# Kernel tuning notes

Hardware: AMD Instinct MI355X
Metric: run time of the kernel (lower is better)

Reference implementation:

```python
import jax, jax.numpy as jnp
import numpy as np

S, B, D, H, L = 1024, 2, 1024, 16, 4
HD = D // H            # 64
MLP = 4 * D            # 4096
EPS = 1e-5


def _ln(x, w, b):
    m = x.mean(-1, keepdims=True)
    v = ((x - m) ** 2).mean(-1, keepdims=True)
    return (x - m) * jax.lax.rsqrt(v + EPS) * w + b


def _rotate_half(x):
    h = x.shape[-1] // 2
    return jnp.concatenate([-x[..., h:], x[..., :h]], axis=-1)


def _rope(t, cos, sin):
    # t: (B, S, H, HD); cos/sin: (S, HD) broadcast to (1, S, 1, HD)
    return t * cos[None, :, None, :] + _rotate_half(t) * sin[None, :, None, :]


def setup_inputs() -> dict:
    key = jax.random.key(0)
    ks = iter(jax.random.split(key, 64))

    def p(shape, scale=0.02):
        return jax.random.normal(next(ks), shape, jnp.float32) * scale

    return {
        "x": jax.random.normal(next(ks), (S, B, D), jnp.float32),
        "rotary_pos_emb": jax.random.normal(next(ks), (S, HD // 2), jnp.float32),
        # stacked per-layer params (leading dim L) for lax.scan
        "ln1_w": jnp.ones((L, D), jnp.float32), "ln1_b": jnp.zeros((L, D), jnp.float32),
        "in_w": p((L, 3 * D, D)), "in_b": jnp.zeros((L, 3 * D), jnp.float32),
        "out_w": p((L, D, D)), "out_b": jnp.zeros((L, D), jnp.float32),
        "ln2_w": jnp.ones((L, D), jnp.float32), "ln2_b": jnp.zeros((L, D), jnp.float32),
        "fc_w": p((L, MLP, D)), "fc_b": jnp.zeros((L, MLP), jnp.float32),
        "cp_w": p((L, D, MLP)), "cp_b": jnp.zeros((L, D), jnp.float32),
        # attention pooling head (qkv_bias=False in CrossAttention)
        "pn_q_w": jnp.ones((D,), jnp.float32), "pn_q_b": jnp.zeros((D,), jnp.float32),
        "pn_k_w": jnp.ones((D,), jnp.float32), "pn_k_b": jnp.zeros((D,), jnp.float32),
        "pn_v_w": jnp.ones((D,), jnp.float32), "pn_v_b": jnp.zeros((D,), jnp.float32),
        "pq_w": p((D, D)), "pk_w": p((D, D)), "pv_w": p((D, D)),
        "pp_w": p((D, D)), "pp_b": jnp.zeros((D,), jnp.float32),
    }


def reference(x, rotary_pos_emb, ln1_w, ln1_b, in_w, in_b, out_w, out_b,
              ln2_w, ln2_b, fc_w, fc_b, cp_w, cp_b,
              pn_q_w, pn_q_b, pn_k_w, pn_k_b, pn_v_w, pn_v_b,
              pq_w, pk_w, pv_w, pp_w, pp_b):
    # freqs (S, HD/2) -> cos/sin tiled twice along last dim: (S, HD)
    cos = jnp.tile(jnp.cos(rotary_pos_emb), (1, 2))
    sin = jnp.tile(jnp.sin(rotary_pos_emb), (1, 2))
    scale = 1.0 / np.sqrt(HD).astype(np.float32)

    def layer(h, p):
        l1w, l1b, iw, ib, ow, ob, l2w, l2b, fw, fb, cw, cb = p
        a = _ln(h, l1w, l1b)
        qkv = jnp.einsum('sbd,ed->sbe', a, iw) + ib           # (S,B,3D)
        qkv = qkv.reshape(S, B, 3, H, HD)
        q = jnp.transpose(qkv[:, :, 0], (1, 0, 2, 3))          # (B,S,H,HD)
        k = jnp.transpose(qkv[:, :, 1], (1, 0, 2, 3))
        v = jnp.transpose(qkv[:, :, 2], (1, 0, 2, 3))
        q = _rope(q, cos, sin)
        k = _rope(k, cos, sin)
        q, k, v = (t.transpose(0, 2, 1, 3) for t in (q, k, v))  # (B,H,S,HD)
        attn = jax.nn.softmax(jnp.einsum('bhsd,bhtd->bhst', q, k) * scale, axis=-1)
        o = jnp.einsum('bhst,bhtd->bhsd', attn, v)
        o = o.transpose(2, 0, 1, 3).reshape(S, B, D)           # back to (S,B,D)
        h = h + jnp.einsum('sbd,ed->sbe', o, ow) + ob          # residual + out_proj
        m = _ln(h, l2w, l2b)
        m = jax.nn.gelu(jnp.einsum('sbd,ed->sbe', m, fw) + fb, approximate=False)
        h = h + jnp.einsum('sbe,de->sbd', m, cw) + cb          # residual + c_proj
        return h, None

    h, _ = jax.lax.scan(layer, x, (ln1_w, ln1_b, in_w, in_b, out_w, out_b,
                                   ln2_w, ln2_b, fc_w, fc_b, cp_w, cp_b))

    # AttentionPoolingBlock: mean-pooled single query, cross-attend over tokens
    t = h.transpose(1, 0, 2)                                   # (B,N,C)
    xq = _ln(t.mean(1, keepdims=True), pn_q_w, pn_q_b)         # (B,1,C)
    xk = _ln(t, pn_k_w, pn_k_b)
    xv = _ln(t, pn_v_w, pn_v_b)
    q = (xq @ pq_w.T).reshape(B, 1, H, HD).transpose(0, 2, 1, 3)   # (B,H,1,HD)
    k = (xk @ pk_w.T).reshape(B, S, H, HD).transpose(0, 2, 1, 3)
    v = (xv @ pv_w.T).reshape(B, S, H, HD).transpose(0, 2, 1, 3)
    a = jax.nn.softmax(jnp.einsum('bhqd,bhtd->bhqt', q, k) * scale, axis=-1)
    o = jnp.einsum('bhqt,bhtd->bhqd', a, v).transpose(0, 2, 1, 3).reshape(B, 1, D)
    return (o @ pp_w.T + pp_b)[:, 0]                           # (B, D)
```

## Files before the change

### kernel.cpp

```cpp
#include <hip/hip_runtime.h>
#include <math.h>

#define S_LEN  1024
#define BATCH  2
#define DMODEL 1024
#define NHEAD  16
#define HDIM   64
#define NLAYER 4
#define MLPD   4096
#define MROWS  (S_LEN*BATCH)

typedef __attribute__((ext_vector_type(8))) short bf16x8_t;
typedef __attribute__((ext_vector_type(4))) float f32x4_t;

__device__ __forceinline__ unsigned short f2bf(float f) {
  union { float f; unsigned u; } c; c.f = f;
  return (unsigned short)((c.u + 0x7FFFu + ((c.u >> 16) & 1u)) >> 16);
}
__device__ __forceinline__ float bf2f(unsigned short u) {
  union { unsigned u; float f; } c; c.u = ((unsigned)u) << 16; return c.f;
}

__device__ __forceinline__ void gl_lds16(const unsigned short* g, unsigned short* l) {
  __builtin_amdgcn_global_load_lds(
      (const __attribute__((address_space(1))) unsigned int*)(g),
      (__attribute__((address_space(3))) unsigned int*)(l), 16, 0, 0);
}

__global__ __launch_bounds__(256) void w2bf_kernel(const float* __restrict__ src,
    unsigned short* __restrict__ dst, int n) {
  const int i = (blockIdx.x * 256 + threadIdx.x) * 8;
  if (i >= n) return;
  float4 v0 = *(const float4*)(src + i);
  float4 v1 = *(const float4*)(src + i + 4);
  ushort4 u0, u1;
  u0.x = f2bf(v0.x); u0.y = f2bf(v0.y); u0.z = f2bf(v0.z); u0.w = f2bf(v0.w);
  u1.x = f2bf(v1.x); u1.y = f2bf(v1.y); u1.z = f2bf(v1.z); u1.w = f2bf(v1.w);
  *(ushort4*)(dst + i)     = u0;
  *(ushort4*)(dst + i + 4) = u1;
}

__global__ __launch_bounds__(256) void trig_kernel(const float* __restrict__ rot,
    float2* __restrict__ tab) {
  const int i = blockIdx.x * 256 + threadIdx.x;
  const float f = rot[i];
  tab[i] = make_float2(cosf(f), sinf(f));
}

template<bool BF16OUT>
__global__ __launch_bounds__(256) void ln_kernel(const float* __restrict__ x,
    const float* __restrict__ w, const float* __restrict__ b,
    void* __restrict__ out, float inscale) {
  const int row = blockIdx.x;
  const int tid = threadIdx.x;
  const float* xr = x + (size_t)row * DMODEL;
  float4 v = *(const float4*)(xr + tid * 4);
  v.x *= inscale; v.y *= inscale; v.z *= inscale; v.w *= inscale;
  float s1 = v.x + v.y + v.z + v.w;
  float s2 = v.x*v.x + v.y*v.y + v.z*v.z + v.w*v.w;
  #pragma unroll
  for (int off = 32; off; off >>= 1) {
    s1 += __shfl_xor(s1, off);
    s2 += __shfl_xor(s2, off);
  }
  __shared__ float as1[4], as2[4];
  if ((tid & 63) == 0) { as1[tid >> 6] = s1; as2[tid >> 6] = s2; }
  __syncthreads();
  s1 = as1[0] + as1[1] + as1[2] + as1[3];
  s2 = as2[0] + as2[1] + as2[2] + as2[3];
  const float mean = s1 * (1.0f / DMODEL);
  const float var  = s2 * (1.0f / DMODEL) - mean * mean;
  const float r = rsqrtf(var + 1e-5f);
  float4 wv = *(const float4*)(w + tid * 4);
  float4 bv = *(const float4*)(b + tid * 4);
  float o0 = (v.x - mean) * r * wv.x + bv.x;
  float o1 = (v.y - mean) * r * wv.y + bv.y;
  float o2 = (v.z - mean) * r * wv.z + bv.z;
  float o3 = (v.w - mean) * r * wv.w + bv.w;
  if (BF16OUT) {
    ushort4 u; u.x = f2bf(o0); u.y = f2bf(o1); u.z = f2bf(o2); u.w = f2bf(o3);
    *(ushort4*)((unsigned short*)out + (size_t)row * DMODEL + tid * 4) = u;
  } else {
    float4 ov; ov.x = o0; ov.y = o1; ov.z = o2; ov.w = o3;
    *(float4*)((float*)out + (size_t)row * DMODEL + tid * 4) = ov;
  }
}

template<int NS, bool ADDDEST, bool DOLN>
__global__ __launch_bounds__(256) void reduce_ln_kernel(
    const float* __restrict__ part, const float* __restrict__ bias,
    float* __restrict__ dest, const float* __restrict__ lnw,
    const float* __restrict__ lnb, unsigned short* __restrict__ lnout) {
  const int row = blockIdx.x;
  const int tid = threadIdx.x;
  const size_t off = (size_t)row * DMODEL + tid * 4;
  float4 v;
  if (ADDDEST) v = *(const float4*)(dest + off);
  else { v.x = 0.f; v.y = 0.f; v.z = 0.f; v.w = 0.f; }
  if (bias) {
    float4 b4 = *(const float4*)(bias + tid * 4);
    v.x += b4.x; v.y += b4.y; v.z += b4.z; v.w += b4.w;
  }
  #pragma unroll
  for (int z = 0; z < NS; ++z) {
    float4 p = *(const float4*)(part + (size_t)z * (MROWS * DMODEL) + off);
    v.x += p.x; v.y += p.y; v.z += p.z; v.w += p.w;
  }
  *(float4*)(dest + off) = v;
  if (DOLN) {
    float s1 = v.x + v.y + v.z + v.w;
    float s2 = v.x*v.x + v.y*v.y + v.z*v.z + v.w*v.w;
    #pragma unroll
    for (int o = 32; o; o >>= 1) {
      s1 += __shfl_xor(s1, o);
      s2 += __shfl_xor(s2, o);
    }
    __shared__ float as1[4], as2[4];
    if ((tid & 63) == 0) { as1[tid >> 6] = s1; as2[tid >> 6] = s2; }
    __syncthreads();
    s1 = as1[0] + as1[1] + as1[2] + as1[3];
    s2 = as2[0] + as2[1] + as2[2] + as2[3];
    const float mean = s1 * (1.0f / DMODEL);
    const float var  = s2 * (1.0f / DMODEL) - mean * mean;
    const float r = rsqrtf(var + 1e-5f);
    float4 wv = *(const float4*)(lnw + tid * 4);
    float4 bv = *(const float4*)(lnb + tid * 4);
    ushort4 u;
    u.x = f2bf((v.x - mean) * r * wv.x + bv.x);
    u.y = f2bf((v.y - mean) * r * wv.y + bv.y);
    u.z = f2bf((v.z - mean) * r * wv.z + bv.z);
    u.w = f2bf((v.w - mean) * r * wv.w + bv.w);
    *(ushort4*)(lnout + (size_t)row * DMODEL + tid * 4) = u;
  }
}

template<int SPLIT, bool GELU, bool PARTIAL, bool OUTBF16>
__global__ __launch_bounds__(256, 3) void gemm_mfma(
    const unsigned short* __restrict__ A, const unsigned short* __restrict__ W,
    const float* __restrict__ bias, void* __restrict__ Cout,
    int M, int N, int K) {
  constexpr int BK = 32;
  __shared__ __align__(16) unsigned short As[3][128 * BK];
  __shared__ __align__(16) unsigned short Bs[3][128 * BK];
  const int tid  = threadIdx.x;
  const int wid  = tid >> 6;
  const int lane = tid & 63;
  const int lrow = lane & 15;
  const int lq   = lane >> 4;

  const int NB = gridDim.x, MB = gridDim.y;
  const int f = blockIdx.y * NB + blockIdx.x;
  const int xcd = f & 7;
  const int idx = f >> 3;
  const int m0 = (idx % MB) * 128;
  const int n0 = (xcd + (idx / MB) * 8) * 128;

  const int wm = (wid >> 1) * 64;
  const int wn = (wid & 1) * 64;
  const int Kc = K / SPLIT;
  const int kbase = blockIdx.z * Kc;
  const int nt = Kc / BK;

  f32x4_t acc[4][4];
  #pragma unroll
  for (int i = 0; i < 4; ++i)
    #pragma unroll
    for (int j = 0; j < 4; ++j) acc[i][j] = (f32x4_t){0.f, 0.f, 0.f, 0.f};

  const int c1 = tid, c2 = tid + 256;
  const unsigned short* Ag1 = A + (size_t)(m0 + (c1 >> 2)) * K + kbase + (c1 & 3) * 8;
  const unsigned short* Ag2 = A + (size_t)(m0 + (c2 >> 2)) * K + kbase + (c2 & 3) * 8;
  const unsigned short* Wg1 = W + (size_t)(n0 + (c1 >> 2)) * K + kbase + (c1 & 3) * 8;
  const unsigned short* Wg2 = W + (size_t)(n0 + (c2 >> 2)) * K + kbase + (c2 & 3) * 8;
  const int l1 = c1 * 8, l2 = c2 * 8;

  auto stage = [&](int t, int b) {
    const int ko = t * BK;
    gl_lds16(Ag1 + ko, &As[b][l1]);
    gl_lds16(Ag2 + ko, &As[b][l2]);
    gl_lds16(Wg1 + ko, &Bs[b][l1]);
    gl_lds16(Wg2 + ko, &Bs[b][l2]);
  };
  auto compute = [&](int b) {
    bf16x8_t af[4], bfr[4];
    #pragma unroll
    for (int i = 0; i < 4; ++i)
      af[i] = *(const bf16x8_t*)&As[b][(wm + i * 16 + lrow) * BK + lq * 8];
    #pragma unroll
    for (int j = 0; j < 4; ++j)
      bfr[j] = *(const bf16x8_t*)&Bs[b][(wn + j * 16 + lrow) * BK + lq * 8];
    #pragma unroll
    for (int i = 0; i < 4; ++i)
      #pragma unroll
      for (int j = 0; j < 4; ++j)
        acc[i][j] = __builtin_amdgcn_mfma_f32_16x16x32_bf16(af[i], bfr[j], acc[i][j], 0, 0, 0);
  };

  stage(0, 0);
  stage(1, 1);

  int cr = 0;
  int cs = 2;
  for (int t = 0; t < nt - 1; ++t) {
    asm volatile("s_waitcnt vmcnt(4)" ::: "memory");
    __builtin_amdgcn_sched_barrier(0);
    __builtin_amdgcn_s_barrier();
    __builtin_amdgcn_sched_barrier(0);
    if (t + 2 < nt) stage(t + 2, cs);
    compute(cr);
    cr = (cr == 2) ? 0 : cr + 1;
    cs = (cs == 2) ? 0 : cs + 1;
  }
  asm volatile("s_waitcnt vmcnt(0)" ::: "memory");
  __builtin_amdgcn_sched_barrier(0);
  __builtin_amdgcn_s_barrier();
  __builtin_amdgcn_sched_barrier(0);
  compute(cr);

  const size_t zoff = PARTIAL ? (size_t)blockIdx.z * ((size_t)M * N) : 0;
  float bj[4];
  #pragma unroll
  for (int j = 0; j < 4; ++j)
    bj[j] = (bias && (SPLIT == 1 || blockIdx.z == 0)) ? bias[n0 + wn + j * 16 + lrow] : 0.f;
  #pragma unroll
  for (int i = 0; i < 4; ++i) {
    #pragma unroll
    for (int r = 0; r < 4; ++r) {
      const int row = m0 + wm + i * 16 + lq * 4 + r;
      const size_t idx2 = (size_t)row * N + n0 + wn + lrow;
      #pragma unroll
      for (int j = 0; j < 4; ++j) {
        float val = acc[i][j][r] + bj[j];
        if (GELU)
          val = 0.5f * val * (1.0f + erff(val * 0.70710678118654752f));
        if (PARTIAL)
          ((float*)Cout)[zoff + idx2 + j * 16] = val;
        else if (OUTBF16)
          ((unsigned short*)Cout)[idx2 + j * 16] = f2bf(val);
        else
          ((float*)Cout)[idx2 + j * 16] = val;
      }
    }
  }
}

__global__ __launch_bounds__(256) void rope_kernel(const unsigned short* __restrict__ qkv,
    const float2* __restrict__ trig, unsigned short* __restrict__ qt,
    unsigned short* __restrict__ kt, unsigned short* __restrict__ vt) {
  const int idx = blockIdx.x * 256 + threadIdx.x;
  const int d  = idx & 63;
  const int hh = (idx >> 6) & 15;
  const int m  = idx >> 10;
  const int s  = m >> 1;
  const int b  = m & 1;
  const float2 t = trig[s * 32 + (d & 31)];
  const float cs = t.x;
  const float sn = t.y;
  const float sign = (d < 32) ? -1.0f : 1.0f;
  const size_t base  = (size_t)m * 3072 + hh * 64;
  const int bh = b * 16 + hh;
  const size_t obase = (((size_t)bh * 1024 + s) << 6) + d;
  float qv = bf2f(qkv[base + d]);
  float qp = bf2f(qkv[base + (d ^ 32)]);
  qt[obase] = f2bf(qv * cs + sign * qp * sn);
  float kv = bf2f(qkv[base + 1024 + d]);
  float kp = bf2f(qkv[base + 1024 + (d ^ 32)]);
  kt[obase] = f2bf(kv * cs + sign * kp * sn);
  vt[(((size_t)bh * 64 + d) << 10) + s] = qkv[base + 2048 + d];
}

__global__ __launch_bounds__(256, 3) void attn_kernel(
    const unsigned short* __restrict__ q, const unsigned short* __restrict__ k,
    const unsigned short* __restrict__ vtr, unsigned short* __restrict__ o) {
  const int tid  = threadIdx.x;
  const int wid  = tid >> 6;
  const int lane = tid & 63;
  const int col  = lane & 15;
  const int quad = lane >> 4;
  const int bh   = blockIdx.x >> 4;
  const int qw   = (blockIdx.x & 15) * 64 + wid * 16;

  __shared__ __align__(16) unsigned short Ks[64 * 72];
  __shared__ __align__(16) unsigned short Vs[64 * 72];
  __shared__ __align__(16) unsigned short Pl_[4][16 * 72];
  unsigned short* Pl = Pl_[wid];

  const unsigned short* kb = k   + ((size_t)bh << 16);
  const unsigned short* vb = vtr + ((size_t)bh << 16);

  bf16x8_t qa0, qa1;
  {
    const unsigned short* qp = q + ((((size_t)bh << 10) + qw + col) << 6) + quad * 8;
    qa0 = *(const bf16x8_t*)(qp);
    qa1 = *(const bf16x8_t*)(qp + 32);
  }

  f32x4_t oacc[4];
  #pragma unroll
  for (int j = 0; j < 4; ++j) oacc[j] = (f32x4_t){0.f, 0.f, 0.f, 0.f};
  float mr[4] = {-3.0e38f, -3.0e38f, -3.0e38f, -3.0e38f};
  float lr[4] = {0.f, 0.f, 0.f, 0.f};

  const int srow = tid >> 2;
  const int scol = (tid & 3) * 16;
  const unsigned short* gk0 = kb + (size_t)srow * 64 + scol;
  const unsigned short* gv0 = vb + (size_t)srow * 1024 + scol;
  unsigned short* lk0 = &Ks[srow * 72 + scol];
  unsigned short* lv0 = &Vs[srow * 72 + scol];

  {
    uint4 ka = *(const uint4*)(gk0);
    uint4 kc = *(const uint4*)(gk0 + 8);
    uint4 va = *(const uint4*)(gv0);
    uint4 vc = *(const uint4*)(gv0 + 8);
    *(uint4*)(lk0)     = ka;
    *(uint4*)(lk0 + 8) = kc;
    *(uint4*)(lv0)     = va;
    *(uint4*)(lv0 + 8) = vc;
  }
  __syncthreads();

  for (int t0 = 0; t0 < 1024; t0 += 64) {
    const bool more = (t0 + 64) < 1024;
    uint4 nka, nkc, nva, nvc;
    if (more) {
      const unsigned short* gk = gk0 + (size_t)(t0 + 64) * 64;
      const unsigned short* gv = gv0 + (t0 + 64);
      nka = *(const uint4*)(gk);
      nkc = *(const uint4*)(gk + 8);
      nva = *(const uint4*)(gv);
      nvc = *(const uint4*)(gv + 8);
    }

    f32x4_t sc[4];
    #pragma unroll
    for (int j = 0; j < 4; ++j) {
      bf16x8_t kf0 = *(const bf16x8_t*)&Ks[(j * 16 + col) * 72 + quad * 8];
      bf16x8_t kf1 = *(const bf16x8_t*)&Ks[(j * 16 + col) * 72 + quad * 8 + 32];
      f32x4_t c = (f32x4_t){0.f, 0.f, 0.f, 0.f};
      c = __builtin_amdgcn_mfma_f32_16x16x32_bf16(qa0, kf0, c, 0, 0, 0);
      c = __builtin_amdgcn_mfma_f32_16x16x32_bf16(qa1, kf1, c, 0, 0, 0);
      sc[j] = c;
    }

    #pragma unroll
    for (int r = 0; r < 4; ++r) {
      float s0 = sc[0][r] * 0.125f, s1 = sc[1][r] * 0.125f;
      float s2 = sc[2][r] * 0.125f, s3 = sc[3][r] * 0.125f;
      float rm = fmaxf(fmaxf(s0, s1), fmaxf(s2, s3));
      rm = fmaxf(rm, __shfl_xor(rm, 1));
      rm = fmaxf(rm, __shfl_xor(rm, 2));
      rm = fmaxf(rm, __shfl_xor(rm, 4));
      rm = fmaxf(rm, __shfl_xor(rm, 8));
      const float mn = fmaxf(mr[r], rm);
      const float alpha = __expf(mr[r] - mn);
      mr[r] = mn;
      const float p0 = __expf(s0 - mn), p1 = __expf(s1 - mn);
      const float p2 = __expf(s2 - mn), p3 = __expf(s3 - mn);
      float rs = p0 + p1 + p2 + p3;
      rs += __shfl_xor(rs, 1);
      rs += __shfl_xor(rs, 2);
      rs += __shfl_xor(rs, 4);
      rs += __shfl_xor(rs, 8);
      lr[r] = lr[r] * alpha + rs;
      #pragma unroll
      for (int j = 0; j < 4; ++j) oacc[j][r] *= alpha;
      const int prow = (quad * 4 + r) * 72;
      Pl[prow +  0 + col] = f2bf(p0);
      Pl[prow + 16 + col] = f2bf(p1);
      Pl[prow + 32 + col] = f2bf(p2);
      Pl[prow + 48 + col] = f2bf(p3);
    }

    bf16x8_t pa0 = *(const bf16x8_t*)&Pl[col * 72 + quad * 8];
    bf16x8_t pa1 = *(const bf16x8_t*)&Pl[col * 72 + quad * 8 + 32];
    #pragma unroll
    for (int j = 0; j < 4; ++j) {
      bf16x8_t vf0 = *(const bf16x8_t*)&Vs[(j * 16 + col) * 72 + quad * 8];
      bf16x8_t vf1 = *(const bf16x8_t*)&Vs[(j * 16 + col) * 72 + quad * 8 + 32];
      oacc[j] = __builtin_amdgcn_mfma_f32_16x16x32_bf16(pa0, vf0, oacc[j], 0, 0, 0);
      oacc[j] = __builtin_amdgcn_mfma_f32_16x16x32_bf16(pa1, vf1, oacc[j], 0, 0, 0);
    }

    __syncthreads();
    if (more) {
      *(uint4*)(lk0)     = nka;
      *(uint4*)(lk0 + 8) = nkc;
      *(uint4*)(lv0)     = nva;
      *(uint4*)(lv0 + 8) = nvc;
    }
    __syncthreads();
  }

  const int b = bh >> 4, hh = bh & 15;
  #pragma unroll
  for (int r = 0; r < 4; ++r) {
    const float inv = 1.0f / lr[r];
    const int sq = qw + quad * 4 + r;
    unsigned short* orow = o + (((size_t)sq * 2 + b) << 10) + hh * 64;
    #pragma unroll
    for (int j = 0; j < 4; ++j)
      orow[j * 16 + col] = f2bf(oacc[j][r] * inv);
  }
}

__global__ __launch_bounds__(256) void mean_kernel(const float* __restrict__ h,
    float* __restrict__ tsum) {
  const int idx = blockIdx.x * 256 + threadIdx.x;
  const int bd = idx & 2047;
  const int sc = idx >> 11;
  const int b = bd >> 10, d = bd & 1023;
  float sm = 0.f;
  for (int s = sc * 128; s < sc * 128 + 128; ++s)
    sm += h[(((size_t)s * 2 + b) << 10) + d];
  atomicAdd(&tsum[bd], sm);
}

__global__ __launch_bounds__(256) void smallmv_kernel(const float* __restrict__ in,
    const float* __restrict__ W, const float* __restrict__ bias,
    float* __restrict__ out) {
  const int lane = threadIdx.x & 63;
  const int n = blockIdx.x * 4 + (threadIdx.x >> 6);
  const int b = blockIdx.y;
  const float* wr = W + (size_t)n * 1024;
  const float* xr = in + (size_t)b * 1024;
  float sm = 0.f;
  #pragma unroll
  for (int j = 0; j < 4; ++j) {
    float4 wv = *(const float4*)(wr + lane * 4 + j * 256);
    float4 xv = *(const float4*)(xr + lane * 4 + j * 256);
    sm += wv.x * xv.x + wv.y * xv.y + wv.z * xv.z + wv.w * xv.w;
  }
  #pragma unroll
  for (int off = 32; off; off >>= 1) sm += __shfl_xor(sm, off);
  if (lane == 0) out[(size_t)b * 1024 + n] = sm + (bias ? bias[n] : 0.f);
}

__global__ __launch_bounds__(256) void pool_attn_part(const float* __restrict__ q,
    const float* __restrict__ k, const float* __restrict__ v,
    float* __restrict__ part) {
  const int wid  = (blockIdx.x * 256 + threadIdx.x) >> 6;
  const int lane = threadIdx.x & 63;
  const int bh = wid >> 4, kblk = wid & 15;
  const int b = bh >> 4, hh = bh & 15;
  const float qd = q[(size_t)b * 1024 + hh * 64 + lane];
  float mx = -3.0e38f, l = 0.f, acc = 0.f;
  for (int t = kblk * 64; t < kblk * 64 + 64; ++t) {
    const size_t ro = (((size_t)t * 2 + b) << 10) + hh * 64 + lane;
    float p = qd * k[ro];
    p += __shfl_xor(p, 32); p += __shfl_xor(p, 16); p += __shfl_xor(p, 8);
    p += __shfl_xor(p, 4);  p += __shfl_xor(p, 2);  p += __shfl_xor(p, 1);
    const float sc = p * 0.125f;
    const float mn = fmaxf(mx, sc);
    const float alpha = __expf(mx - mn);
    const float w = __expf(sc - mn);
    acc = acc * alpha + w * v[ro];
    l   = l * alpha + w;
    mx  = mn;
  }
  float* pp = part + (size_t)wid * 68;
  if (lane == 0) { pp[0] = mx; pp[1] = l; }
  pp[4 + lane] = acc;
}

__global__ __launch_bounds__(256) void pool_attn_comb(const float* __restrict__ part,
    float* __restrict__ o) {
  const int wid  = (blockIdx.x * 256 + threadIdx.x) >> 6;
  const int lane = threadIdx.x & 63;
  const float* pb = part + (size_t)wid * 16 * 68;
  float M = -3.0e38f;
  #pragma unroll
  for (int w = 0; w < 16; ++w) M = fmaxf(M, pb[w * 68]);
  float L = 0.f, O = 0.f;
  #pragma unroll
  for (int w = 0; w < 16; ++w) {
    const float e = __expf(pb[w * 68] - M);
    L += e * pb[w * 68 + 1];
    O += e * pb[w * 68 + 4 + lane];
  }
  const int b = wid >> 4, hh = wid & 15;
  o[(size_t)b * 1024 + hh * 64 + lane] = O / L;
}

extern "C" void kernel_launch(void* const* d_in, const int* in_sizes, int n_in,
                              void* d_out, int out_size, void* d_ws, size_t ws_size,
                              hipStream_t stream) {
  (void)in_sizes; (void)n_in; (void)out_size; (void)ws_size;
  const float* x     = (const float*)d_in[0];
  const float* rot   = (const float*)d_in[1];
  const float* ln1_w = (const float*)d_in[2];
  const float* ln1_b = (const float*)d_in[3];
  const float* in_w  = (const float*)d_in[4];
  const float* in_b  = (const float*)d_in[5];
  const float* out_w = (const float*)d_in[6];
  const float* out_b = (const float*)d_in[7];
  const float* ln2_w = (const float*)d_in[8];
  const float* ln2_b = (const float*)d_in[9];
  const float* fc_w  = (const float*)d_in[10];
  const float* fc_b  = (const float*)d_in[11];
  const float* cp_w  = (const float*)d_in[12];
  const float* cp_b  = (const float*)d_in[13];
  const float* pn_q_w = (const float*)d_in[14];
  const float* pn_q_b = (const float*)d_in[15];
  const float* pn_k_w = (const float*)d_in[16];
  const float* pn_k_b = (const float*)d_in[17];
  const float* pn_v_w = (const float*)d_in[18];
  const float* pn_v_b = (const float*)d_in[19];
  const float* pq_w  = (const float*)d_in[20];
  const float* pk_w  = (const float*)d_in[21];
  const float* pv_w  = (const float*)d_in[22];
  const float* pp_w  = (const float*)d_in[23];
  const float* pp_b  = (const float*)d_in[24];

  float* ws = (float*)d_ws;
  const size_t M1 = 1u << 20;
  float* h  = ws;
  float* a  = ws + 2 * M1;
  float* r1 = ws + 4 * M1;
  float* qt = ws + 12 * M1;
  float* kt = ws + 14 * M1;
  float* vt = ws + 16 * M1;
  float* o  = ws + 18 * M1;
  float* trig = ws + 19 * M1;
  float* wbf = ws + 20 * M1;
  unsigned short* a_bf  = (unsigned short*)a;
  unsigned short* r1_bf = (unsigned short*)r1;
  unsigned short* o_bf  = (unsigned short*)o;
  unsigned short* qt_bf = (unsigned short*)qt;
  unsigned short* kt_bf = (unsigned short*)kt;
  unsigned short* vt_bf = (unsigned short*)vt;
  unsigned short* wb_qkv = (unsigned short*)wbf;
  unsigned short* wb_out = wb_qkv + 3145728;
  unsigned short* wb_fc  = wb_out + 1048576;
  unsigned short* wb_cp  = wb_fc  + 4194304;
  float* part_op = r1;
  float* part_cp = qt;
  float* part_pool = ws + 5 * M1;
  float* tsum  = qt;
  float* xq    = qt + 2048;
  float* qpool = qt + 4096;
  float* opool = qt + 6144;
  float* ppart = qt + 8192;

  hipMemcpyAsync(h, x, 2 * M1 * sizeof(float), hipMemcpyDeviceToDevice, stream);

  trig_kernel<<<128, 256, 0, stream>>>(rot, (float2*)trig);
  ln_kernel<true><<<MROWS, 256, 0, stream>>>(h, ln1_w, ln1_b, a_bf, 1.0f);

  for (int l = 0; l < NLAYER; ++l) {
    w2bf_kernel<<<3145728 / 2048, 256, 0, stream>>>(in_w + (size_t)l * 3145728, wb_qkv, 3145728);
    w2bf_kernel<<<1048576 / 2048, 256, 0, stream>>>(out_w + (size_t)l * 1048576, wb_out, 1048576);
    w2bf_kernel<<<4194304 / 2048, 256, 0, stream>>>(fc_w + (size_t)l * 4194304, wb_fc, 4194304);
    w2bf_kernel<<<4194304 / 2048, 256, 0, stream>>>(cp_w + (size_t)l * 4194304, wb_cp, 4194304);

    gemm_mfma<1, false, false, true><<<dim3(3072 / 128, MROWS / 128, 1), 256, 0, stream>>>(
        a_bf, wb_qkv, in_b + l * 3072, r1_bf, MROWS, 3072, 1024);
    rope_kernel<<<8192, 256, 0, stream>>>(r1_bf, (const float2*)trig, qt_bf, kt_bf, vt_bf);
    attn_kernel<<<512, 256, 0, stream>>>(qt_bf, kt_bf, vt_bf, o_bf);
    gemm_mfma<4, false, true, false><<<dim3(1024 / 128, MROWS / 128, 4), 256, 0, stream>>>(
        o_bf, wb_out, nullptr, part_op, MROWS, 1024, 1024);
    reduce_ln_kernel<4, true, true><<<MROWS, 256, 0, stream>>>(
        part_op, out_b + l * 1024, h, ln2_w + l * DMODEL, ln2_b + l * DMODEL, a_bf);
    gemm_mfma<1, true, false, true><<<dim3(4096 / 128, MROWS / 128, 1), 256, 0, stream>>>(
        a_bf, wb_fc, fc_b + l * 4096, r1_bf, MROWS, 4096, 1024);
    gemm_mfma<4, false, true, false><<<dim3(1024 / 128, MROWS / 128, 4), 256, 0, stream>>>(
        r1_bf, wb_cp, nullptr, part_cp, MROWS, 1024, 4096);
    if (l < NLAYER - 1)
      reduce_ln_kernel<4, true, true><<<MROWS, 256, 0, stream>>>(
          part_cp, cp_b + l * 1024, h,
          ln1_w + (l + 1) * DMODEL, ln1_b + (l + 1) * DMODEL, a_bf);
    else
      reduce_ln_kernel<4, true, false><<<MROWS, 256, 0, stream>>>(
          part_cp, cp_b + l * 1024, h, nullptr, nullptr, nullptr);
  }

  hipMemsetAsync(tsum, 0, 2048 * sizeof(float), stream);
  mean_kernel<<<64, 256, 0, stream>>>(h, tsum);
  ln_kernel<false><<<BATCH, 256, 0, stream>>>(tsum, pn_q_w, pn_q_b, xq, 1.0f / S_LEN);
  ln_kernel<true><<<MROWS, 256, 0, stream>>>(h, pn_k_w, pn_k_b, a_bf, 1.0f);
  ln_kernel<true><<<MROWS, 256, 0, stream>>>(h, pn_v_w, pn_v_b, r1_bf, 1.0f);
  smallmv_kernel<<<dim3(256, BATCH), 256, 0, stream>>>(xq, pq_w, nullptr, qpool);
  w2bf_kernel<<<1048576 / 2048, 256, 0, stream>>>(pk_w, wb_qkv, 1048576);
  w2bf_kernel<<<1048576 / 2048, 256, 0, stream>>>(pv_w, wb_out, 1048576);
  gemm_mfma<2, false, true, false><<<dim3(1024 / 128, MROWS / 128, 2), 256, 0, stream>>>(
      a_bf, wb_qkv, nullptr, part_pool, MROWS, 1024, 1024);
  reduce_ln_kernel<2, false, false><<<MROWS, 256, 0, stream>>>(
      part_pool, nullptr, kt, nullptr, nullptr, nullptr);
  gemm_mfma<2, false, true, false><<<dim3(1024 / 128, MROWS / 128, 2), 256, 0, stream>>>(
      r1_bf, wb_out, nullptr, part_pool, MROWS, 1024, 1024);
  reduce_ln_kernel<2, false, false><<<MROWS, 256, 0, stream>>>(
      part_pool, nullptr, vt, nullptr, nullptr, nullptr);
  pool_attn_part<<<128, 256, 0, stream>>>(qpool, kt, vt, ppart);
  pool_attn_comb<<<8, 256, 0, stream>>>(ppart, opool);
  smallmv_kernel<<<dim3(256, BATCH), 256, 0, stream>>>(opool, pp_w, pp_b, (float*)d_out);
}
```

Measured before the change: 1.085 ms.

## Transpose V via LDS-tiled kernel and use DPP reductions with lazy softmax rescale

Moves the V transpose out of the rope kernel into a dedicated kernel that stages a 64x64 tile in shared memory, so global writes are coalesced instead of strided 2-byte scatters. In the attention softmax, the cross-lane shuffles for row max and sum become DPP row operations. The running-max rescale of the accumulators is skipped when no lane's max increased. The cost is one extra kernel launch per layer.

Result: faster. 1.059 ms (-2.4%).

```diff
diff --git a/kernel.cpp b/kernel.cpp
--- a/kernel.cpp
+++ b/kernel.cpp
@@ -25,6 +25,26 @@
   __builtin_amdgcn_global_load_lds(
       (const __attribute__((address_space(1))) unsigned int*)(g),
       (__attribute__((address_space(3))) unsigned int*)(l), 16, 0, 0);
+}
+
+template<int CTRL>
+__device__ __forceinline__ float dpp16(float x) {
+  return __int_as_float(__builtin_amdgcn_update_dpp(
+      0, __float_as_int(x), CTRL, 0xf, 0xf, true));
+}
+__device__ __forceinline__ float rowmax16(float x) {
+  x = fmaxf(x, dpp16<0x128>(x));
+  x = fmaxf(x, dpp16<0x124>(x));
+  x = fmaxf(x, dpp16<0x122>(x));
+  x = fmaxf(x, dpp16<0x121>(x));
+  return x;
+}
+__device__ __forceinline__ float rowsum16(float x) {
+  x += dpp16<0x128>(x);
+  x += dpp16<0x124>(x);
+  x += dpp16<0x122>(x);
+  x += dpp16<0x121>(x);
+  return x;
 }
 
 __global__ __launch_bounds__(256) void w2bf_kernel(const float* __restrict__ src,
@@ -246,7 +266,7 @@
 
 __global__ __launch_bounds__(256) void rope_kernel(const unsigned short* __restrict__ qkv,
     const float2* __restrict__ trig, unsigned short* __restrict__ qt,
-    unsigned short* __restrict__ kt, unsigned short* __restrict__ vt) {
+    unsigned short* __restrict__ kt) {
   const int idx = blockIdx.x * 256 + threadIdx.x;
   const int d  = idx & 63;
   const int hh = (idx >> 6) & 15;
@@ -266,7 +286,29 @@
   float kv = bf2f(qkv[base + 1024 + d]);
   float kp = bf2f(qkv[base + 1024 + (d ^ 32)]);
   kt[obase] = f2bf(kv * cs + sign * kp * sn);
-  vt[(((size_t)bh * 64 + d) << 10) + s] = qkv[base + 2048 + d];
+}
+
+__global__ __launch_bounds__(256) void vtrans_kernel(const unsigned short* __restrict__ qkv,
+    unsigned short* __restrict__ vt) {
+  const int bh = blockIdx.x >> 4;
+  const int s0 = (blockIdx.x & 15) * 64;
+  const int b = bh >> 4, hh = bh & 15;
+  __shared__ unsigned short Vl[64 * 72];
+  const int t = threadIdx.x;
+  const int sl = t >> 2, dcol = (t & 3) * 16;
+  const unsigned short* src = qkv + (size_t)((s0 + sl) * 2 + b) * 3072 + 2048 + hh * 64 + dcol;
+  uint4 a = *(const uint4*)(src);
+  uint4 c = *(const uint4*)(src + 8);
+  *(uint4*)&Vl[sl * 72 + dcol]     = a;
+  *(uint4*)&Vl[sl * 72 + dcol + 8] = c;
+  __syncthreads();
+  const int dr = t >> 2, soff = (t & 3) * 16;
+  unsigned short o[16];
+  #pragma unroll
+  for (int i = 0; i < 16; ++i) o[i] = Vl[(soff + i) * 72 + dr];
+  unsigned short* dst = vt + (((size_t)bh * 64 + dr) << 10) + s0 + soff;
+  *(uint4*)(dst)     = *(uint4*)(o);
+  *(uint4*)(dst + 8) = *(uint4*)(o + 8);
 }
 
 __global__ __launch_bounds__(256, 3) void attn_kernel(
@@ -347,24 +389,19 @@
     for (int r = 0; r < 4; ++r) {
       float s0 = sc[0][r] * 0.125f, s1 = sc[1][r] * 0.125f;
       float s2 = sc[2][r] * 0.125f, s3 = sc[3][r] * 0.125f;
-      float rm = fmaxf(fmaxf(s0, s1), fmaxf(s2, s3));
-      rm = fmaxf(rm, __shfl_xor(rm, 1));
-      rm = fmaxf(rm, __shfl_xor(rm, 2));
-      rm = fmaxf(rm, __shfl_xor(rm, 4));
-      rm = fmaxf(rm, __shfl_xor(rm, 8));
-      const float mn = fmaxf(mr[r], rm);
-      const float alpha = __expf(mr[r] - mn);
-      mr[r] = mn;
-      const float p0 = __expf(s0 - mn), p1 = __expf(s1 - mn);
-      const float p2 = __expf(s2 - mn), p3 = __expf(s3 - mn);
-      float rs = p0 + p1 + p2 + p3;
-      rs += __shfl_xor(rs, 1);
-      rs += __shfl_xor(rs, 2);
-      rs += __shfl_xor(rs, 4);
-      rs += __shfl_xor(rs, 8);
-      lr[r] = lr[r] * alpha + rs;
-      #pragma unroll
-      for (int j = 0; j < 4; ++j) oacc[j][r] *= alpha;
+      const float rm = rowmax16(fmaxf(fmaxf(s0, s1), fmaxf(s2, s3)));
+      if (__any(rm > mr[r])) {
+        const float mn = fmaxf(mr[r], rm);
+        const float alpha = __expf(mr[r] - mn);
+        mr[r] = mn;
+        lr[r] *= alpha;
+        #pragma unroll
+        for (int j = 0; j < 4; ++j) oacc[j][r] *= alpha;
+      }
+      const float m = mr[r];
+      const float p0 = __expf(s0 - m), p1 = __expf(s1 - m);
+      const float p2 = __expf(s2 - m), p3 = __expf(s3 - m);
+      lr[r] += rowsum16(p0 + p1 + p2 + p3);
       const int prow = (quad * 4 + r) * 72;
       Pl[prow +  0 + col] = f2bf(p0);
       Pl[prow + 16 + col] = f2bf(p1);
@@ -555,7 +592,8 @@
 
     gemm_mfma<1, false, false, true><<<dim3(3072 / 128, MROWS / 128, 1), 256, 0, stream>>>(
         a_bf, wb_qkv, in_b + l * 3072, r1_bf, MROWS, 3072, 1024);
-    rope_kernel<<<8192, 256, 0, stream>>>(r1_bf, (const float2*)trig, qt_bf, kt_bf, vt_bf);
+    rope_kernel<<<8192, 256, 0, stream>>>(r1_bf, (const float2*)trig, qt_bf, kt_bf);
+    vtrans_kernel<<<512, 256, 0, stream>>>(r1_bf, vt_bf);
     attn_kernel<<<512, 256, 0, stream>>>(qt_bf, kt_bf, vt_bf, o_bf);
     gemm_mfma<4, false, true, false><<<dim3(1024 / 128, MROWS / 128, 4), 256, 0, stream>>>(
         o_bf, wb_out, nullptr, part_op, MROWS, 1024, 1024);
```
